# Kernel tuning notes

Hardware: AMD Instinct MI355X
Metric: run time of the kernel (lower is better)

Reference implementation:

```python
import jax, jax.numpy as jnp
import numpy as np

M, K, N = 32, 4096, 12288


def setup_inputs() -> dict:
    key = jax.random.key(0)
    k1, k2, k3, k4 = jax.random.split(key, 4)
    x = jax.random.normal(k1, (M, K), dtype=jnp.float32)
    # uint8-valued packed weight (stored as int32 for harness compatibility, values in [0,256))
    weight_u8 = jax.random.randint(k2, (K, N), 0, 256, dtype=jnp.int32)
    # per-output-channel fp16 scale and zero-point
    scale = (jax.random.uniform(k3, (N,), dtype=jnp.float32) * 0.01 + 1e-3).astype(jnp.float16)
    zero = (jax.random.uniform(k4, (N,), dtype=jnp.float32) * 255.0).astype(jnp.float16)
    return {"x": x, "weight_u8": weight_u8, "scale": scale, "zero": zero}


def reference(x, weight_u8, scale, zero):
    # QuantMatmulCustom: dequantize uint8 weight with per-channel fp16 scale/zero, then matmul.
    # w_deq[k, n] = (w_u8[k, n] - zero[n]) * scale[n]
    w_deq = (weight_u8.astype(jnp.float32) - zero.astype(jnp.float32)[None, :]) * scale.astype(jnp.float32)[None, :]
    # [M, K] @ [K, N] -> [M, N]
    return jnp.einsum('mk,kn->mn', x, w_deq)
```

## Files before the change

kernel.cpp:

```cpp
#include <hip/hip_runtime.h>

#define M_DIM 32
#define K_DIM 4096
#define N_DIM 12288
#define SPLITK 16
#define KPER  (K_DIM / SPLITK)
#define NT    (KPER / 32)
#define BLK   512
#define NPB   128
#define DBUF  4

using bf16x8 = __attribute__((ext_vector_type(8))) short;
using f32x4  = __attribute__((ext_vector_type(4))) float;

typedef __attribute__((address_space(1))) const void GASV;
typedef __attribute__((address_space(3))) void LASV;

__device__ __forceinline__ bf16x8 pack_b(const int (&wv)[8]) {
    union { unsigned u[4]; bf16x8 v; } r;
    #pragma unroll
    for (int p = 0; p < 4; ++p) {
        unsigned a = __float_as_uint((float)wv[2 * p]);
        unsigned b = __float_as_uint((float)wv[2 * p + 1]);
        r.u[p] = __builtin_amdgcn_perm(b, a, 0x07060302);
    }
    return r.v;
}

template <bool WS>
__global__ __launch_bounds__(BLK, 4) void qmm_main(const float* __restrict__ x,
                                                   const int* __restrict__ w,
                                                   float* __restrict__ dst) {
    __shared__ short lds_a[NT * 2 * 64 * 8];
    __shared__ int   lds_b[8 * DBUF * 512];

    const int tid  = threadIdx.x;
    const int lane = tid & 63;
    const int g    = lane >> 4;
    const int c    = lane & 15;
    const int wid  = tid >> 6;
    const int k0   = blockIdx.y * KPER;
    const int n0   = blockIdx.x * NPB;
    const int n0w  = n0 + wid * 16;

    const int* gsrc[2];
    #pragma unroll
    for (int q = 0; q < 2; ++q) {
        const int r  = 16 * q + (lane >> 2);
        const int cg = (lane & 3) ^ ((r >> 3) & 3);
        gsrc[q] = w + (size_t)(k0 + r) * N_DIM + n0w + 4 * cg;
    }
    int* const ldst = &lds_b[wid * (DBUF * 512)];

#define ISSUE(T) do {                                                          \
    __builtin_amdgcn_sched_barrier(0);                                         \
    __builtin_amdgcn_global_load_lds((GASV*)(gsrc[0] + (size_t)32 * (T) * N_DIM), \
        (LASV*)(ldst + ((T) & 3) * 512),       16, 0, 0);                      \
    __builtin_amdgcn_global_load_lds((GASV*)(gsrc[1] + (size_t)32 * (T) * N_DIM), \
        (LASV*)(ldst + ((T) & 3) * 512 + 256), 16, 0, 0);                      \
} while (0)

#define WAITV(N) do { asm volatile("s_waitcnt vmcnt(" #N ")" ::: "memory");    \
    __builtin_amdgcn_sched_barrier(0); } while (0)

    ISSUE(0); ISSUE(1); ISSUE(2); ISSUE(3);

    for (int s = tid; s < NT * 2 * 64; s += BLK) {
        const int l  = s & 63;
        const int h  = (s >> 6) & 1;
        const int kt = s >> 7;
        const int m  = 16 * h + (l & 15);
        const float* xp = x + (size_t)m * K_DIM + k0 + kt * 32 + 8 * (l >> 4);
        bf16x8 v;
        #pragma unroll
        for (int j = 0; j < 8; ++j) {
            unsigned u = __float_as_uint(xp[j]);
            u += 0x7FFFu + ((u >> 16) & 1u);
            v[j] = (short)(u >> 16);
        }
        *(bf16x8*)&lds_a[s * 8] = v;
    }
    __syncthreads();

    bf16x8 areg[NT * 2];
    {
        const short* la = lds_a + lane * 8;
        #pragma unroll
        for (int i = 0; i < NT * 2; ++i)
            areg[i] = *(const bf16x8*)&la[(size_t)i * 512];
    }

    const int* brd = lds_b + wid * (DBUF * 512) + 128 * g + 4 * ((c >> 2) ^ g) + (c & 3);

    f32x4 acc0 = {0.f, 0.f, 0.f, 0.f};
    f32x4 acc1 = {0.f, 0.f, 0.f, 0.f};

#define COMP(T) do {                                                           \
    int wv[8];                                                                 \
    _Pragma("unroll")                                                          \
    for (int j = 0; j < 8; ++j) wv[j] = brd[((T) & 3) * 512 + j * 16];         \
    bf16x8 bfv = pack_b(wv);                                                   \
    acc0 = __builtin_amdgcn_mfma_f32_16x16x32_bf16(areg[2*(T)],   bfv, acc0, 0, 0, 0); \
    acc1 = __builtin_amdgcn_mfma_f32_16x16x32_bf16(areg[2*(T)+1], bfv, acc1, 0, 0, 0); \
} while (0)

    COMP(0); ISSUE(4);
    COMP(1); ISSUE(5);
    COMP(2); ISSUE(6);
    COMP(3); ISSUE(7);
    WAITV(6); COMP(4);
    WAITV(4); COMP(5);
    WAITV(2); COMP(6);
    WAITV(0); COMP(7);

#undef ISSUE
#undef WAITV
#undef COMP

    if (WS) {
        float* pp = dst + ((size_t)blockIdx.y * M_DIM) * N_DIM + n0w + c;
        #pragma unroll
        for (int i = 0; i < 4; ++i) {
            const int r = 4 * (lane >> 4) + i;
            pp[(size_t)r * N_DIM]        = acc0[i];
            pp[(size_t)(16 + r) * N_DIM] = acc1[i];
        }
    } else {
        #pragma unroll
        for (int i = 0; i < 4; ++i) {
            const int r = 4 * (lane >> 4) + i;
            atomicAdd(&dst[(size_t)r * N_DIM + n0w + c], acc0[i]);
            atomicAdd(&dst[(size_t)(16 + r) * N_DIM + n0w + c], acc1[i]);
        }
    }
}

__global__ __launch_bounds__(256) void qmm_rowsum(const float* __restrict__ x,
                                                  float* __restrict__ rowsum) {
    const int m = blockIdx.x;
    __shared__ float red[256];
    const float4* xp = (const float4*)(x + (size_t)m * K_DIM);
    float s = 0.f;
    #pragma unroll
    for (int i = 0; i < K_DIM / 4 / 256; ++i) {
        float4 v = xp[threadIdx.x + 256 * i];
        s += v.x + v.y + v.z + v.w;
    }
    red[threadIdx.x] = s;
    __syncthreads();
    #pragma unroll
    for (int off = 128; off > 0; off >>= 1) {
        if (threadIdx.x < off) red[threadIdx.x] += red[threadIdx.x + off];
        __syncthreads();
    }
    if (threadIdx.x == 0) rowsum[m] = red[0];
}

__global__ __launch_bounds__(256) void qmm_finalize(const float* __restrict__ part,
                                                    const float* __restrict__ rowsum,
                                                    const float* __restrict__ scale,
                                                    const float* __restrict__ zero,
                                                    float* __restrict__ out) {
    const int m  = blockIdx.y;
    const int n4 = blockIdx.x * 256 + threadIdx.x;
    const float rs = rowsum[m];
    float4 acc = make_float4(0.f, 0.f, 0.f, 0.f);
    #pragma unroll
    for (int sp = 0; sp < SPLITK; ++sp) {
        float4 p = ((const float4*)(part + ((size_t)sp * M_DIM + m) * N_DIM))[n4];
        acc.x += p.x; acc.y += p.y; acc.z += p.z; acc.w += p.w;
    }
    const float4 sc = ((const float4*)scale)[n4];
    const float4 zp = ((const float4*)zero)[n4];
    float4 o;
    o.x = sc.x * (acc.x - zp.x * rs);
    o.y = sc.y * (acc.y - zp.y * rs);
    o.z = sc.z * (acc.z - zp.z * rs);
    o.w = sc.w * (acc.w - zp.w * rs);
    ((float4*)(out + (size_t)m * N_DIM))[n4] = o;
}

__global__ __launch_bounds__(256) void qmm_zero(float* __restrict__ out) {
    int i = blockIdx.x * 256 + threadIdx.x;
    ((float4*)out)[i] = make_float4(0.f, 0.f, 0.f, 0.f);
}
__global__ __launch_bounds__(256) void qmm_scale(const float* __restrict__ x,
                                                 const float* __restrict__ scale,
                                                 const float* __restrict__ zero,
                                                 float* __restrict__ out) {
    const int m = blockIdx.y;
    __shared__ float red[256];
    float s = 0.f;
    for (int k = threadIdx.x; k < K_DIM; k += 256)
        s += x[(size_t)m * K_DIM + k];
    red[threadIdx.x] = s;
    __syncthreads();
    #pragma unroll
    for (int off = 128; off > 0; off >>= 1) {
        if (threadIdx.x < off) red[threadIdx.x] += red[threadIdx.x + off];
        __syncthreads();
    }
    const float rowsum = red[0];
    const int n = blockIdx.x * 256 + threadIdx.x;
    const float v = out[(size_t)m * N_DIM + n];
    out[(size_t)m * N_DIM + n] = scale[n] * (v - zero[n] * rowsum);
}

extern "C" void kernel_launch(void* const* d_in, const int* in_sizes, int n_in,
                              void* d_out, int out_size, void* d_ws, size_t ws_size,
                              hipStream_t stream) {
    const float* x     = (const float*)d_in[0];
    const int*   w     = (const int*)d_in[1];
    const float* scale = (const float*)d_in[2];
    const float* zero  = (const float*)d_in[3];
    float* out = (float*)d_out;

    const size_t part_sz = (size_t)SPLITK * M_DIM * N_DIM * sizeof(float);
    const size_t need    = part_sz + M_DIM * sizeof(float);
    if (ws_size >= need) {
        float* part   = (float*)d_ws;
        float* rowsum = (float*)((char*)d_ws + part_sz);
        qmm_main<true><<<dim3(N_DIM / NPB, SPLITK), dim3(BLK), 0, stream>>>(x, w, part);
        qmm_rowsum    <<<dim3(M_DIM),               dim3(256), 0, stream>>>(x, rowsum);
        qmm_finalize  <<<dim3(N_DIM / 4 / 256, M_DIM), dim3(256), 0, stream>>>(part, rowsum, scale, zero, out);
    } else {
        qmm_zero <<<dim3((M_DIM * N_DIM / 4) / 256),  dim3(256), 0, stream>>>(out);
        qmm_main<false><<<dim3(N_DIM / NPB, SPLITK),  dim3(BLK), 0, stream>>>(x, w, out);
        qmm_scale<<<dim3(N_DIM / 256, M_DIM),         dim3(256), 0, stream>>>(x, scale, zero, out);
    }
}
```

Baseline: 45.73 us.

## Precompute bf16 A fragments once, halve split-K, and stream A with weights

Adds a prep kernel that converts x to bf16 MFMA fragments once and computes the row sums, replacing the separate rowsum kernel. The main kernel then loads A fragments from global memory alongside each weight tile instead of having every block convert its x slice to LDS. Split-K drops from 16 to 8, giving 16 k-tiles per block with a steady double-buffered LDS pipeline. LDS bank swizzling is replaced by an even/odd pair swap baked into the A fragments. The aim is to remove redundant per-block conversion and reduce partial-sum traffic, at the cost of fewer blocks and an extra launch on the critical path.

```diff
diff --git a/kernel.cpp b/kernel.cpp
--- a/kernel.cpp
+++ b/kernel.cpp
@@ -3,18 +3,23 @@
 #define M_DIM 32
 #define K_DIM 4096
 #define N_DIM 12288
-#define SPLITK 16
+#define SPLITK 8
 #define KPER  (K_DIM / SPLITK)
 #define NT    (KPER / 32)
 #define BLK   512
 #define NPB   128
-#define DBUF  4
 
 using bf16x8 = __attribute__((ext_vector_type(8))) short;
 using f32x4  = __attribute__((ext_vector_type(4))) float;
 
 typedef __attribute__((address_space(1))) const void GASV;
 typedef __attribute__((address_space(3))) void LASV;
+
+__device__ __forceinline__ short to_bf16(float f) {
+    unsigned u = __float_as_uint(f);
+    u += 0x7FFFu + ((u >> 16) & 1u);
+    return (short)(u >> 16);
+}
 
 __device__ __forceinline__ bf16x8 pack_b(const int (&wv)[8]) {
     union { unsigned u[4]; bf16x8 v; } r;
@@ -27,91 +32,127 @@
     return r.v;
 }
 
+__global__ __launch_bounds__(256) void qmm_prep(const float* __restrict__ x,
+                                                short* __restrict__ frag,
+                                                float* __restrict__ rowsum) {
+    const int b   = blockIdx.x;
+    const int tid = threadIdx.x;
+
+    __shared__ float red[256];
+    const float4* xr = (const float4*)(x + (size_t)b * K_DIM);
+    float s = 0.f;
+    #pragma unroll
+    for (int i = 0; i < K_DIM / 4 / 256; ++i) {
+        float4 v = xr[tid + 256 * i];
+        s += v.x + v.y + v.z + v.w;
+    }
+    red[tid] = s;
+    __syncthreads();
+    #pragma unroll
+    for (int off = 128; off > 0; off >>= 1) {
+        if (tid < off) red[tid] += red[tid + off];
+        __syncthreads();
+    }
+    if (tid == 0) rowsum[b] = red[0];
+
+    #pragma unroll
+    for (int i = 0; i < 2; ++i) {
+        const int s2   = i * 256 + tid;
+        const int kt   = 4 * b + (s2 >> 7);
+        const int h    = (s2 >> 6) & 1;
+        const int lane = s2 & 63;
+        const int g    = lane >> 4;
+        const int g0   = g & 1;
+        const int m    = 16 * h + (lane & 15);
+        const float* xp = x + (size_t)m * K_DIM + kt * 32 + 8 * g;
+        float p0 = xp[0], p1 = xp[1], p2 = xp[2], p3 = xp[3];
+        float p4 = xp[4], p5 = xp[5], p6 = xp[6], p7 = xp[7];
+        bf16x8 v;
+        v[0] = to_bf16(g0 ? p1 : p0);  v[1] = to_bf16(g0 ? p0 : p1);
+        v[2] = to_bf16(g0 ? p3 : p2);  v[3] = to_bf16(g0 ? p2 : p3);
+        v[4] = to_bf16(g0 ? p5 : p4);  v[5] = to_bf16(g0 ? p4 : p5);
+        v[6] = to_bf16(g0 ? p7 : p6);  v[7] = to_bf16(g0 ? p6 : p7);
+        *(bf16x8*)&frag[(size_t)((kt * 2 + h) * 64 + lane) * 8] = v;
+    }
+}
+
 template <bool WS>
-__global__ __launch_bounds__(BLK, 4) void qmm_main(const float* __restrict__ x,
+__global__ __launch_bounds__(BLK, 4) void qmm_main(const short* __restrict__ frag,
                                                    const int* __restrict__ w,
                                                    float* __restrict__ dst) {
-    __shared__ short lds_a[NT * 2 * 64 * 8];
-    __shared__ int   lds_b[8 * DBUF * 512];
+    __shared__ int lds_b[8 * 2 * 512];
 
     const int tid  = threadIdx.x;
     const int lane = tid & 63;
     const int g    = lane >> 4;
+    const int g0   = g & 1;
     const int c    = lane & 15;
     const int wid  = tid >> 6;
     const int k0   = blockIdx.y * KPER;
-    const int n0   = blockIdx.x * NPB;
-    const int n0w  = n0 + wid * 16;
+    const int n0w  = blockIdx.x * NPB + wid * 16;
 
     const int* gsrc[2];
     #pragma unroll
-    for (int q = 0; q < 2; ++q) {
-        const int r  = 16 * q + (lane >> 2);
-        const int cg = (lane & 3) ^ ((r >> 3) & 3);
-        gsrc[q] = w + (size_t)(k0 + r) * N_DIM + n0w + 4 * cg;
-    }
-    int* const ldst = &lds_b[wid * (DBUF * 512)];
-
-#define ISSUE(T) do {                                                          \
-    __builtin_amdgcn_sched_barrier(0);                                         \
-    __builtin_amdgcn_global_load_lds((GASV*)(gsrc[0] + (size_t)32 * (T) * N_DIM), \
-        (LASV*)(ldst + ((T) & 3) * 512),       16, 0, 0);                      \
-    __builtin_amdgcn_global_load_lds((GASV*)(gsrc[1] + (size_t)32 * (T) * N_DIM), \
-        (LASV*)(ldst + ((T) & 3) * 512 + 256), 16, 0, 0);                      \
-} while (0)
-
-#define WAITV(N) do { asm volatile("s_waitcnt vmcnt(" #N ")" ::: "memory");    \
-    __builtin_amdgcn_sched_barrier(0); } while (0)
-
-    ISSUE(0); ISSUE(1); ISSUE(2); ISSUE(3);
-
-    for (int s = tid; s < NT * 2 * 64; s += BLK) {
-        const int l  = s & 63;
-        const int h  = (s >> 6) & 1;
-        const int kt = s >> 7;
-        const int m  = 16 * h + (l & 15);
-        const float* xp = x + (size_t)m * K_DIM + k0 + kt * 32 + 8 * (l >> 4);
-        bf16x8 v;
-        #pragma unroll
-        for (int j = 0; j < 8; ++j) {
-            unsigned u = __float_as_uint(xp[j]);
-            u += 0x7FFFu + ((u >> 16) & 1u);
-            v[j] = (short)(u >> 16);
-        }
-        *(bf16x8*)&lds_a[s * 8] = v;
-    }
-    __syncthreads();
-
-    bf16x8 areg[NT * 2];
-    {
-        const short* la = lds_a + lane * 8;
-        #pragma unroll
-        for (int i = 0; i < NT * 2; ++i)
-            areg[i] = *(const bf16x8*)&la[(size_t)i * 512];
-    }
-
-    const int* brd = lds_b + wid * (DBUF * 512) + 128 * g + 4 * ((c >> 2) ^ g) + (c & 3);
+    for (int q = 0; q < 2; ++q)
+        gsrc[q] = w + (size_t)(k0 + 16 * q + (lane >> 2)) * N_DIM + n0w + 4 * (lane & 3);
+
+    int* const wbase = &lds_b[wid * 1024];
+
+    const int vb = 4 * (128 * g + 4 * (c >> 2) + (c & 3));
+    const int be = vb + 64 * g0;
+    const int bo = vb + 64 * (1 - g0);
+
+    const short* asrc = frag + ((size_t)(blockIdx.y * NT) * 1024 + lane * 8);
 
     f32x4 acc0 = {0.f, 0.f, 0.f, 0.f};
     f32x4 acc1 = {0.f, 0.f, 0.f, 0.f};
-
-#define COMP(T) do {                                                           \
-    int wv[8];                                                                 \
-    _Pragma("unroll")                                                          \
-    for (int j = 0; j < 8; ++j) wv[j] = brd[((T) & 3) * 512 + j * 16];         \
-    bf16x8 bfv = pack_b(wv);                                                   \
-    acc0 = __builtin_amdgcn_mfma_f32_16x16x32_bf16(areg[2*(T)],   bfv, acc0, 0, 0, 0); \
-    acc1 = __builtin_amdgcn_mfma_f32_16x16x32_bf16(areg[2*(T)+1], bfv, acc1, 0, 0, 0); \
+    bf16x8 aA0, aA1, aB0, aB1;
+
+#define ISSUE(T) do {                                                            \
+    __builtin_amdgcn_sched_barrier(0);                                           \
+    __builtin_amdgcn_global_load_lds((GASV*)(gsrc[0] + (size_t)(32 * (T)) * N_DIM), \
+        (LASV*)(wbase + ((T) & 1) * 512),       16, 0, 0);                       \
+    __builtin_amdgcn_global_load_lds((GASV*)(gsrc[1] + (size_t)(32 * (T)) * N_DIM), \
+        (LASV*)(wbase + ((T) & 1) * 512 + 256), 16, 0, 0);                       \
+    if ((T) & 1) { aB0 = *(const bf16x8*)(asrc + (T) * 1024);                    \
+                   aB1 = *(const bf16x8*)(asrc + (T) * 1024 + 512); }            \
+    else         { aA0 = *(const bf16x8*)(asrc + (T) * 1024);                    \
+                   aA1 = *(const bf16x8*)(asrc + (T) * 1024 + 512); }            \
+    __builtin_amdgcn_sched_barrier(0);                                           \
 } while (0)
 
-    COMP(0); ISSUE(4);
-    COMP(1); ISSUE(5);
-    COMP(2); ISSUE(6);
-    COMP(3); ISSUE(7);
-    WAITV(6); COMP(4);
-    WAITV(4); COMP(5);
-    WAITV(2); COMP(6);
-    WAITV(0); COMP(7);
+#define WAITV(N) do { asm volatile("s_waitcnt vmcnt(" #N ")" ::: "memory");      \
+    __builtin_amdgcn_sched_barrier(0); } while (0)
+
+#define COMP(T) do {                                                             \
+    char* pb = (char*)wbase + ((T) & 1) * 2048;                                  \
+    int wv[8];                                                                   \
+    wv[0] = *(int*)(pb + be);        wv[1] = *(int*)(pb + bo);                   \
+    wv[2] = *(int*)(pb + be + 128);  wv[3] = *(int*)(pb + bo + 128);             \
+    wv[4] = *(int*)(pb + be + 256);  wv[5] = *(int*)(pb + bo + 256);             \
+    wv[6] = *(int*)(pb + be + 384);  wv[7] = *(int*)(pb + bo + 384);             \
+    bf16x8 bfv = pack_b(wv);                                                     \
+    acc0 = __builtin_amdgcn_mfma_f32_16x16x32_bf16(((T) & 1) ? aB0 : aA0, bfv, acc0, 0, 0, 0); \
+    acc1 = __builtin_amdgcn_mfma_f32_16x16x32_bf16(((T) & 1) ? aB1 : aA1, bfv, acc1, 0, 0, 0); \
+} while (0)
+
+    ISSUE(0); ISSUE(1);
+    WAITV(4); COMP(0);  ISSUE(2);
+    WAITV(4); COMP(1);  ISSUE(3);
+    WAITV(4); COMP(2);  ISSUE(4);
+    WAITV(4); COMP(3);  ISSUE(5);
+    WAITV(4); COMP(4);  ISSUE(6);
+    WAITV(4); COMP(5);  ISSUE(7);
+    WAITV(4); COMP(6);  ISSUE(8);
+    WAITV(4); COMP(7);  ISSUE(9);
+    WAITV(4); COMP(8);  ISSUE(10);
+    WAITV(4); COMP(9);  ISSUE(11);
+    WAITV(4); COMP(10); ISSUE(12);
+    WAITV(4); COMP(11); ISSUE(13);
+    WAITV(4); COMP(12); ISSUE(14);
+    WAITV(4); COMP(13); ISSUE(15);
+    WAITV(4); COMP(14);
+    WAITV(0); COMP(15);
 
 #undef ISSUE
 #undef WAITV
@@ -135,27 +176,6 @@
     }
 }
 
-__global__ __launch_bounds__(256) void qmm_rowsum(const float* __restrict__ x,
-                                                  float* __restrict__ rowsum) {
-    const int m = blockIdx.x;
-    __shared__ float red[256];
-    const float4* xp = (const float4*)(x + (size_t)m * K_DIM);
-    float s = 0.f;
-    #pragma unroll
-    for (int i = 0; i < K_DIM / 4 / 256; ++i) {
-        float4 v = xp[threadIdx.x + 256 * i];
-        s += v.x + v.y + v.z + v.w;
-    }
-    red[threadIdx.x] = s;
-    __syncthreads();
-    #pragma unroll
-    for (int off = 128; off > 0; off >>= 1) {
-        if (threadIdx.x < off) red[threadIdx.x] += red[threadIdx.x + off];
-        __syncthreads();
-    }
-    if (threadIdx.x == 0) rowsum[m] = red[0];
-}
-
 __global__ __launch_bounds__(256) void qmm_finalize(const float* __restrict__ part,
                                                     const float* __restrict__ rowsum,
                                                     const float* __restrict__ scale,
@@ -215,17 +235,20 @@
     const float* zero  = (const float*)d_in[3];
     float* out = (float*)d_out;
 
+    const size_t frag_sz = (size_t)128 * 2 * 64 * 8 * sizeof(short);
     const size_t part_sz = (size_t)SPLITK * M_DIM * N_DIM * sizeof(float);
-    const size_t need    = part_sz + M_DIM * sizeof(float);
-    if (ws_size >= need) {
-        float* part   = (float*)d_ws;
-        float* rowsum = (float*)((char*)d_ws + part_sz);
-        qmm_main<true><<<dim3(N_DIM / NPB, SPLITK), dim3(BLK), 0, stream>>>(x, w, part);
-        qmm_rowsum    <<<dim3(M_DIM),               dim3(256), 0, stream>>>(x, rowsum);
-        qmm_finalize  <<<dim3(N_DIM / 4 / 256, M_DIM), dim3(256), 0, stream>>>(part, rowsum, scale, zero, out);
+    short* fragp  = (short*)d_ws;
+    float* rowsum = (float*)((char*)d_ws + frag_sz);
+    float* part   = (float*)((char*)d_ws + frag_sz + 256);
+
+    if (ws_size >= frag_sz + 256 + part_sz) {
+        qmm_prep    <<<dim3(32),                 dim3(256), 0, stream>>>(x, fragp, rowsum);
+        qmm_main<true><<<dim3(N_DIM / NPB, SPLITK), dim3(BLK), 0, stream>>>(fragp, w, part);
+        qmm_finalize<<<dim3(N_DIM / 4 / 256, M_DIM), dim3(256), 0, stream>>>(part, rowsum, scale, zero, out);
     } else {
-        qmm_zero <<<dim3((M_DIM * N_DIM / 4) / 256),  dim3(256), 0, stream>>>(out);
-        qmm_main<false><<<dim3(N_DIM / NPB, SPLITK),  dim3(BLK), 0, stream>>>(x, w, out);
-        qmm_scale<<<dim3(N_DIM / 256, M_DIM),         dim3(256), 0, stream>>>(x, scale, zero, out);
-    }
-}
+        qmm_prep    <<<dim3(32),                 dim3(256), 0, stream>>>(x, fragp, rowsum);
+        qmm_zero    <<<dim3((M_DIM * N_DIM / 4) / 256), dim3(256), 0, stream>>>(out);
+        qmm_main<false><<<dim3(N_DIM / NPB, SPLITK), dim3(BLK), 0, stream>>>(fragp, w, out);
+        qmm_scale   <<<dim3(N_DIM / 256, M_DIM), dim3(256), 0, stream>>>(x, scale, zero, out);
+    }
+}
```

After: 46.00 us. About the same (+0.6%).
